# Kernel tuning notes

Hardware: AMD Instinct MI355X
Metric: run time of the kernel (lower is better)

## Reference

```python
import jax, jax.numpy as jnp
import numpy as np

B, NR, IC, NC, OC = 64, 16384, 16, 10, 16
NUM_ITERS = 3


def setup_inputs() -> dict:
    key = jax.random.key(0)
    k1, k2, k3, k4 = jax.random.split(key, 4)
    x = jax.random.normal(k1, (B, NR, IC), dtype=jnp.float32)
    W = jax.random.normal(k2, (IC, NC, OC, NR), dtype=jnp.float32)
    fc_w = jax.random.normal(k3, (1, NC * OC), dtype=jnp.float32)
    fc_b = jax.random.normal(k4, (1,), dtype=jnp.float32)
    return {"x": x, "W": W, "fc_w": fc_w, "fc_b": fc_b}


def _squash(s):
    # Original squash is applied to tensors with trailing dim of size 1,
    # so the norm reduction is elementwise: s^2 * s / ((1+s^2) * sqrt(s^2))
    sq = s * s
    return sq * s / ((1.0 + sq) * jnp.sqrt(sq))


def reference(x, W, fc_w, fc_b):
    batch = x.shape[0]
    in_ch, nc, oc, nr = W.shape
    # u_hat[b,i,c,o] = sum_r W[i,c,o,r] * x[b,r,i]  (x is identical across capsules)
    u_hat = jnp.einsum('icor,bri->bico', W, x)  # [B, in_ch, nc, oc]
    b_ij = jnp.zeros((in_ch, nc), dtype=x.dtype)
    v_j = None
    for it in range(NUM_ITERS):
        c_ij = jax.nn.softmax(b_ij, axis=0)              # softmax over in_channels
        s_j = jnp.einsum('ic,bico->bco', c_ij, u_hat)    # [B, nc, oc]
        v_j = _squash(s_j)
        if it < NUM_ITERS - 1:
            # agreement a[b,i,c] = sum_o u_hat[b,i,c,o] * v[b,c,o]; mean over batch
            a_ij = jnp.einsum('bico,bco->ic', u_hat, v_j) / batch
            b_ij = b_ij + a_ij
    pred = jax.nn.sigmoid(v_j.reshape(batch, -1) @ fc_w.T + fc_b)[:, 0]  # [B]
    return pred, v_j[..., None]  # v_j returned as [B, nc, oc, 1] like torch
```

## Files before the change

kernel.cpp:

```cpp
#include <hip/hip_runtime.h>

typedef unsigned int uint;
typedef unsigned short ushort;
typedef __attribute__((ext_vector_type(8))) short bf16x8;
typedef __attribute__((ext_vector_type(4))) float floatx4;
typedef __attribute__((ext_vector_type(4))) uint uint4v;

#define B_   64
#define NR_  16384
#define IC_  16
#define NC_  10
#define OC_  16
#define NCO  160
#define KC_  32
#define KT_  32

__device__ __forceinline__ float bf2f(ushort h) {
    return __uint_as_float(((uint)h) << 16);
}
__device__ __forceinline__ ushort f2bf(float f) {
    uint u = __float_as_uint(f);
    u += 0x7fffu + ((u >> 16) & 1u);
    return (ushort)(u >> 16);
}
__device__ __forceinline__ void splitbf(float f, ushort& h, ushort& l) {
    h = f2bf(f);
    l = f2bf(f - bf2f(h));
}
__device__ __forceinline__ float squashf(float s) {
    return s * fabsf(s) / (1.0f + s * s);
}

__global__ __launch_bounds__(256) void k_xT(const float* __restrict__ xf,
                                            ushort* __restrict__ xTh,
                                            ushort* __restrict__ xTl)
{
    const int chunk = blockIdx.x, b = blockIdx.y, t = threadIdx.x;
    const int r0 = chunk * 1024;
#pragma unroll
    for (int j = 0; j < 4; ++j) {
        int r = r0 + t + 256 * j;
        const float* row = xf + ((size_t)b * NR_ + r) * IC_;
        float vals[16];
        *(float4*)&vals[0]  = *(const float4*)row;
        *(float4*)&vals[4]  = *(const float4*)(row + 4);
        *(float4*)&vals[8]  = *(const float4*)(row + 8);
        *(float4*)&vals[12] = *(const float4*)(row + 12);
#pragma unroll
        for (int i = 0; i < 16; ++i) {
            ushort h, l;
            splitbf(vals[i], h, l);
            size_t idx = ((size_t)(i * B_ + b)) * NR_ + r;
            xTh[idx] = h;
            xTl[idx] = l;
        }
    }
}

__global__ __launch_bounds__(512) void k_uhat(const float* __restrict__ xf,
                                              const float* __restrict__ wf,
                                              const ushort* __restrict__ xTh,
                                              const ushort* __restrict__ xTl,
                                              int has_xt,
                                              float* __restrict__ uh)
{
    const int i    = blockIdx.x;
    const int kc   = blockIdx.y;
    const int tid  = threadIdx.x;
    const int lane = tid & 63;
    const int w    = tid >> 6;
    const int quad = lane >> 4;
    const int m16  = lane & 15;
    const int bt   = w & 3;
    const int cg   = w >> 2;

    __shared__ ushort Xh[64 * 40], Xl[64 * 40];
    __shared__ ushort Wh[160 * 40], Wl[160 * 40];

    floatx4 acc[5];
#pragma unroll
    for (int t = 0; t < 5; ++t) acc[t] = (floatx4){0.f, 0.f, 0.f, 0.f};

    const int r0 = kc * (NR_ / KC_);

    for (int st = 0; st < (NR_ / KC_) / KT_; ++st) {
        const int rb = r0 + st * KT_;
        __syncthreads();
        if (has_xt) {
            int t8 = tid & 255, bb = t8 >> 2, part = t8 & 3;
            size_t src = (size_t)(i * B_ + bb) * NR_ + rb + part * 8;
            if (tid < 256)
                *(uint4v*)&Xh[bb * 40 + part * 8] = *(const uint4v*)&xTh[src];
            else
                *(uint4v*)&Xl[bb * 40 + part * 8] = *(const uint4v*)&xTl[src];
        } else {
#pragma unroll
            for (int s = 0; s < 4; ++s) {
                int n = tid + 512 * s;
                int bb = n >> 5, k = n & 31;
                float v = xf[(size_t)bb * (NR_ * IC_) + (size_t)(rb + k) * IC_ + i];
                ushort h, l;
                splitbf(v, h, l);
                Xh[bb * 40 + k] = h;
                Xl[bb * 40 + k] = l;
            }
        }
        for (int j = tid; j < 640; j += 512) {
            int row = j >> 2, seg = j & 3;
            const float* wp = wf + (size_t)(i * NCO + row) * NR_ + rb + seg * 8;
            float4 f0 = *(const float4*)wp;
            float4 f1 = *(const float4*)(wp + 4);
            float v[8] = {f0.x, f0.y, f0.z, f0.w, f1.x, f1.y, f1.z, f1.w};
            ushort hh[8], ll[8];
#pragma unroll
            for (int q = 0; q < 8; ++q) splitbf(v[q], hh[q], ll[q]);
            uint4v ph, pl;
#pragma unroll
            for (int q = 0; q < 4; ++q) {
                ph[q] = (uint)hh[2 * q] | ((uint)hh[2 * q + 1] << 16);
                pl[q] = (uint)ll[2 * q] | ((uint)ll[2 * q + 1] << 16);
            }
            *(uint4v*)&Wh[row * 40 + seg * 8] = ph;
            *(uint4v*)&Wl[row * 40 + seg * 8] = pl;
        }
        __syncthreads();
        bf16x8 afh = *(const bf16x8*)&Xh[(bt * 16 + m16) * 40 + quad * 8];
        bf16x8 afl = *(const bf16x8*)&Xl[(bt * 16 + m16) * 40 + quad * 8];
#pragma unroll
        for (int t = 0; t < 5; ++t) {
            int corow = (cg * 5 + t) * 16 + m16;
            bf16x8 bh = *(const bf16x8*)&Wh[corow * 40 + quad * 8];
            bf16x8 bl = *(const bf16x8*)&Wl[corow * 40 + quad * 8];
            acc[t] = __builtin_amdgcn_mfma_f32_16x16x32_bf16(afh, bh, acc[t], 0, 0, 0);
            acc[t] = __builtin_amdgcn_mfma_f32_16x16x32_bf16(afl, bh, acc[t], 0, 0, 0);
            acc[t] = __builtin_amdgcn_mfma_f32_16x16x32_bf16(afh, bl, acc[t], 0, 0, 0);
        }
    }
#pragma unroll
    for (int t = 0; t < 5; ++t) {
        int co = (cg * 5 + t) * 16 + m16;
#pragma unroll
        for (int r = 0; r < 4; ++r) {
            int b = bt * 16 + quad * 4 + r;
            atomicAdd(&uh[(b * IC_ + i) * NCO + co], acc[t][r]);
        }
    }
}

__global__ __launch_bounds__(256) void k_route1(const float* __restrict__ uh,
                                                float* __restrict__ a1)
{
    const int b = blockIdx.x, tid = threadIdx.x;
    __shared__ float vL[NCO];
    const float* ub = uh + b * IC_ * NCO;
    if (tid < NCO) {
        float s = 0.f;
#pragma unroll
        for (int i = 0; i < IC_; ++i) s += ub[i * NCO + tid];
        vL[tid] = squashf(s * (1.0f / 16.0f));
    }
    __syncthreads();
    if (tid < NCO) {
        int i = tid / NC_, c = tid - i * NC_;
        float sum = 0.f;
#pragma unroll
        for (int o = 0; o < OC_; ++o)
            sum += ub[i * NCO + c * OC_ + o] * vL[c * OC_ + o];
        atomicAdd(&a1[i * NC_ + c], sum * (1.0f / 64.0f));
    }
}

__global__ __launch_bounds__(256) void k_route2(const float* __restrict__ uh,
                                                const float* __restrict__ a1,
                                                float* __restrict__ a2)
{
    const int b = blockIdx.x, tid = threadIdx.x;
    __shared__ float aL[NCO];
    __shared__ float vL[NCO];
    if (tid < NCO) aL[tid] = a1[tid];
    __syncthreads();
    const float* ub = uh + b * IC_ * NCO;
    if (tid < NCO) {
        int c = tid >> 4;
        float m = -1e30f;
        for (int i = 0; i < IC_; ++i) m = fmaxf(m, aL[i * NC_ + c]);
        float Z = 0.f;
        for (int i = 0; i < IC_; ++i) Z += expf(aL[i * NC_ + c] - m);
        float s = 0.f;
        for (int i = 0; i < IC_; ++i)
            s += (expf(aL[i * NC_ + c] - m) / Z) * ub[i * NCO + tid];
        vL[tid] = squashf(s);
    }
    __syncthreads();
    if (tid < NCO) {
        int i = tid / NC_, c = tid - i * NC_;
        float sum = 0.f;
#pragma unroll
        for (int o = 0; o < OC_; ++o)
            sum += ub[i * NCO + c * OC_ + o] * vL[c * OC_ + o];
        atomicAdd(&a2[i * NC_ + c], sum * (1.0f / 64.0f));
    }
}

__global__ __launch_bounds__(256) void k_route3(const float* __restrict__ uh,
                                                const float* __restrict__ a1,
                                                const float* __restrict__ a2,
                                                const float* __restrict__ fcw,
                                                const float* __restrict__ fcb,
                                                float* __restrict__ out)
{
    const int b = blockIdx.x, tid = threadIdx.x;
    __shared__ float bL[NCO];
    __shared__ float pL[NCO];
    if (tid < NCO) bL[tid] = a1[tid] + a2[tid];
    __syncthreads();
    const float* ub = uh + b * IC_ * NCO;
    if (tid < NCO) {
        int c = tid >> 4;
        float m = -1e30f;
        for (int i = 0; i < IC_; ++i) m = fmaxf(m, bL[i * NC_ + c]);
        float Z = 0.f;
        for (int i = 0; i < IC_; ++i) Z += expf(bL[i * NC_ + c] - m);
        float s = 0.f;
        for (int i = 0; i < IC_; ++i)
            s += (expf(bL[i * NC_ + c] - m) / Z) * ub[i * NCO + tid];
        float v = squashf(s);
        out[64 + b * NCO + tid] = v;
        pL[tid] = v * fcw[tid];
    }
    __syncthreads();
    if (tid == 0) {
        float accv = fcb[0];
        for (int j = 0; j < NCO; ++j) accv += pL[j];
        out[b] = 1.0f / (1.0f + expf(-accv));
    }
}

extern "C" void kernel_launch(void* const* d_in, const int* in_sizes, int n_in,
                              void* d_out, int out_size, void* d_ws, size_t ws_size,
                              hipStream_t stream)
{
    const float* x   = (const float*)d_in[0];
    const float* W   = (const float*)d_in[1];
    const float* fcw = (const float*)d_in[2];
    const float* fcb = (const float*)d_in[3];
    float* out = (float*)d_out;

    float* uh = (float*)d_ws;
    float* a1 = uh + B_ * IC_ * NCO;
    float* a2 = a1 + NCO;
    const size_t xt_off   = 1u << 20;
    const size_t xt_bytes = (size_t)IC_ * B_ * NR_ * 2;
    ushort* xTh = (ushort*)((char*)d_ws + xt_off);
    ushort* xTl = (ushort*)((char*)d_ws + xt_off + xt_bytes);
    const int has_xt = (ws_size >= xt_off + 2 * xt_bytes) ? 1 : 0;

    hipMemsetAsync(d_ws, 0, (size_t)(B_ * IC_ * NCO + 2 * NCO) * sizeof(float), stream);
    if (has_xt)
        k_xT<<<dim3(16, 64), 256, 0, stream>>>(x, xTh, xTl);
    k_uhat<<<dim3(IC_, KC_), 512, 0, stream>>>(x, W, xTh, xTl, has_xt, uh);
    k_route1<<<B_, 256, 0, stream>>>(uh, a1);
    k_route2<<<B_, 256, 0, stream>>>(uh, a1, a2);
    k_route3<<<B_, 256, 0, stream>>>(uh, a1, a2, fcw, fcb, out);
}
```

Baseline: 320.6 us.

## Replace atomics with partial-sum buffers, widen K tile, vectorize transpose

The u_hat GEMM now writes per-K-chunk partial results to a workspace buffer, and a new reduce kernel sums them instead of using global atomicAdd. The hipMemset is removed. The K tile doubles to 64 with padded shared-memory strides, which halves the loop iterations and barriers. The x transpose kernel now loads four rows per thread and stores packed 8-byte values. The routing kernels stage u_hat in shared memory and compute per-batch agreement partials that are summed on read rather than with atomics. The fallback path for small workspaces is dropped, so the code now assumes a larger workspace (over 100 MB) is available.

New measurement: 324.1 us. Within noise of the previous version (+1.1%).

```diff
diff --git a/kernel.cpp b/kernel.cpp
--- a/kernel.cpp
+++ b/kernel.cpp
@@ -5,6 +5,7 @@
 typedef __attribute__((ext_vector_type(8))) short bf16x8;
 typedef __attribute__((ext_vector_type(4))) float floatx4;
 typedef __attribute__((ext_vector_type(4))) uint uint4v;
+typedef __attribute__((ext_vector_type(2))) uint uint2v;
 
 #define B_   64
 #define NR_  16384
@@ -12,8 +13,9 @@
 #define NC_  10
 #define OC_  16
 #define NCO  160
+#define ICO  2560
 #define KC_  32
-#define KT_  32
+#define KT_  64
 
 __device__ __forceinline__ float bf2f(ushort h) {
     return __uint_as_float(((uint)h) << 16);
@@ -36,33 +38,31 @@
                                             ushort* __restrict__ xTl)
 {
     const int chunk = blockIdx.x, b = blockIdx.y, t = threadIdx.x;
-    const int r0 = chunk * 1024;
-#pragma unroll
-    for (int j = 0; j < 4; ++j) {
-        int r = r0 + t + 256 * j;
-        const float* row = xf + ((size_t)b * NR_ + r) * IC_;
-        float vals[16];
-        *(float4*)&vals[0]  = *(const float4*)row;
-        *(float4*)&vals[4]  = *(const float4*)(row + 4);
-        *(float4*)&vals[8]  = *(const float4*)(row + 8);
-        *(float4*)&vals[12] = *(const float4*)(row + 12);
-#pragma unroll
-        for (int i = 0; i < 16; ++i) {
-            ushort h, l;
-            splitbf(vals[i], h, l);
-            size_t idx = ((size_t)(i * B_ + b)) * NR_ + r;
-            xTh[idx] = h;
-            xTl[idx] = l;
-        }
-    }
-}
-
-__global__ __launch_bounds__(512) void k_uhat(const float* __restrict__ xf,
-                                              const float* __restrict__ wf,
+    const int r0 = chunk * 1024 + t * 4;
+    const float* base = xf + ((size_t)b * NR_ + r0) * IC_;
+    float v[4][16];
+#pragma unroll
+    for (int q = 0; q < 4; ++q)
+#pragma unroll
+        for (int s = 0; s < 4; ++s)
+            *(float4*)&v[q][s * 4] = *(const float4*)(base + q * IC_ + s * 4);
+#pragma unroll
+    for (int i = 0; i < 16; ++i) {
+        ushort h[4], l[4];
+#pragma unroll
+        for (int q = 0; q < 4; ++q) splitbf(v[q][i], h[q], l[q]);
+        size_t idx = ((size_t)(i * B_ + b)) * NR_ + r0;
+        *(uint2v*)&xTh[idx] = (uint2v){(uint)h[0] | ((uint)h[1] << 16),
+                                       (uint)h[2] | ((uint)h[3] << 16)};
+        *(uint2v*)&xTl[idx] = (uint2v){(uint)l[0] | ((uint)l[1] << 16),
+                                       (uint)l[2] | ((uint)l[3] << 16)};
+    }
+}
+
+__global__ __launch_bounds__(512) void k_uhat(const float* __restrict__ wf,
                                               const ushort* __restrict__ xTh,
                                               const ushort* __restrict__ xTl,
-                                              int has_xt,
-                                              float* __restrict__ uh)
+                                              float* __restrict__ up)
 {
     const int i    = blockIdx.x;
     const int kc   = blockIdx.y;
@@ -74,8 +74,8 @@
     const int bt   = w & 3;
     const int cg   = w >> 2;
 
-    __shared__ ushort Xh[64 * 40], Xl[64 * 40];
-    __shared__ ushort Wh[160 * 40], Wl[160 * 40];
+    __shared__ ushort Xh[64 * 72], Xl[64 * 72];
+    __shared__ ushort Wh[160 * 72], Wl[160 * 72];
 
     floatx4 acc[5];
 #pragma unroll
@@ -86,27 +86,14 @@
     for (int st = 0; st < (NR_ / KC_) / KT_; ++st) {
         const int rb = r0 + st * KT_;
         __syncthreads();
-        if (has_xt) {
-            int t8 = tid & 255, bb = t8 >> 2, part = t8 & 3;
-            size_t src = (size_t)(i * B_ + bb) * NR_ + rb + part * 8;
-            if (tid < 256)
-                *(uint4v*)&Xh[bb * 40 + part * 8] = *(const uint4v*)&xTh[src];
-            else
-                *(uint4v*)&Xl[bb * 40 + part * 8] = *(const uint4v*)&xTl[src];
-        } else {
-#pragma unroll
-            for (int s = 0; s < 4; ++s) {
-                int n = tid + 512 * s;
-                int bb = n >> 5, k = n & 31;
-                float v = xf[(size_t)bb * (NR_ * IC_) + (size_t)(rb + k) * IC_ + i];
-                ushort h, l;
-                splitbf(v, h, l);
-                Xh[bb * 40 + k] = h;
-                Xl[bb * 40 + k] = l;
-            }
-        }
-        for (int j = tid; j < 640; j += 512) {
-            int row = j >> 2, seg = j & 3;
+        {
+            int bb = tid >> 3, seg = tid & 7;
+            size_t src = (size_t)(i * B_ + bb) * NR_ + rb + seg * 8;
+            *(uint4v*)&Xh[bb * 72 + seg * 8] = *(const uint4v*)&xTh[src];
+            *(uint4v*)&Xl[bb * 72 + seg * 8] = *(const uint4v*)&xTl[src];
+        }
+        for (int j = tid; j < 1280; j += 512) {
+            int row = j >> 3, seg = j & 7;
             const float* wp = wf + (size_t)(i * NCO + row) * NR_ + rb + seg * 8;
             float4 f0 = *(const float4*)wp;
             float4 f1 = *(const float4*)(wp + 4);
@@ -120,20 +107,23 @@
                 ph[q] = (uint)hh[2 * q] | ((uint)hh[2 * q + 1] << 16);
                 pl[q] = (uint)ll[2 * q] | ((uint)ll[2 * q + 1] << 16);
             }
-            *(uint4v*)&Wh[row * 40 + seg * 8] = ph;
-            *(uint4v*)&Wl[row * 40 + seg * 8] = pl;
+            *(uint4v*)&Wh[row * 72 + seg * 8] = ph;
+            *(uint4v*)&Wl[row * 72 + seg * 8] = pl;
         }
         __syncthreads();
-        bf16x8 afh = *(const bf16x8*)&Xh[(bt * 16 + m16) * 40 + quad * 8];
-        bf16x8 afl = *(const bf16x8*)&Xl[(bt * 16 + m16) * 40 + quad * 8];
-#pragma unroll
-        for (int t = 0; t < 5; ++t) {
-            int corow = (cg * 5 + t) * 16 + m16;
-            bf16x8 bh = *(const bf16x8*)&Wh[corow * 40 + quad * 8];
-            bf16x8 bl = *(const bf16x8*)&Wl[corow * 40 + quad * 8];
-            acc[t] = __builtin_amdgcn_mfma_f32_16x16x32_bf16(afh, bh, acc[t], 0, 0, 0);
-            acc[t] = __builtin_amdgcn_mfma_f32_16x16x32_bf16(afl, bh, acc[t], 0, 0, 0);
-            acc[t] = __builtin_amdgcn_mfma_f32_16x16x32_bf16(afh, bl, acc[t], 0, 0, 0);
+#pragma unroll
+        for (int kk = 0; kk < 2; ++kk) {
+            bf16x8 afh = *(const bf16x8*)&Xh[(bt * 16 + m16) * 72 + kk * 32 + quad * 8];
+            bf16x8 afl = *(const bf16x8*)&Xl[(bt * 16 + m16) * 72 + kk * 32 + quad * 8];
+#pragma unroll
+            for (int t = 0; t < 5; ++t) {
+                int corow = (cg * 5 + t) * 16 + m16;
+                bf16x8 bh = *(const bf16x8*)&Wh[corow * 72 + kk * 32 + quad * 8];
+                bf16x8 bl = *(const bf16x8*)&Wl[corow * 72 + kk * 32 + quad * 8];
+                acc[t] = __builtin_amdgcn_mfma_f32_16x16x32_bf16(afh, bh, acc[t], 0, 0, 0);
+                acc[t] = __builtin_amdgcn_mfma_f32_16x16x32_bf16(afl, bh, acc[t], 0, 0, 0);
+                acc[t] = __builtin_amdgcn_mfma_f32_16x16x32_bf16(afh, bl, acc[t], 0, 0, 0);
+            }
         }
     }
 #pragma unroll
@@ -142,21 +132,33 @@
 #pragma unroll
         for (int r = 0; r < 4; ++r) {
             int b = bt * 16 + quad * 4 + r;
-            atomicAdd(&uh[(b * IC_ + i) * NCO + co], acc[t][r]);
-        }
-    }
-}
-
-__global__ __launch_bounds__(256) void k_route1(const float* __restrict__ uh,
-                                                float* __restrict__ a1)
+            up[((size_t)kc * B_ + b) * ICO + i * NCO + co] = acc[t][r];
+        }
+    }
+}
+
+__global__ __launch_bounds__(256) void k_reduce(const float* __restrict__ up,
+                                                float* __restrict__ uh)
+{
+    const int g = blockIdx.x * 256 + threadIdx.x;
+    float s = 0.f;
+#pragma unroll
+    for (int kc = 0; kc < KC_; ++kc) s += up[(size_t)kc * (B_ * ICO) + g];
+    uh[g] = s;
+}
+
+__global__ __launch_bounds__(256) void k_r1(const float* __restrict__ uh,
+                                            float* __restrict__ a1p)
 {
     const int b = blockIdx.x, tid = threadIdx.x;
+    __shared__ float uhb[ICO];
     __shared__ float vL[NCO];
-    const float* ub = uh + b * IC_ * NCO;
-    if (tid < NCO) {
-        float s = 0.f;
-#pragma unroll
-        for (int i = 0; i < IC_; ++i) s += ub[i * NCO + tid];
+    for (int e = tid; e < ICO; e += 256) uhb[e] = uh[b * ICO + e];
+    __syncthreads();
+    if (tid < NCO) {
+        float s = 0.f;
+#pragma unroll
+        for (int i = 0; i < IC_; ++i) s += uhb[i * NCO + tid];
         vL[tid] = squashf(s * (1.0f / 16.0f));
     }
     __syncthreads();
@@ -165,21 +167,27 @@
         float sum = 0.f;
 #pragma unroll
         for (int o = 0; o < OC_; ++o)
-            sum += ub[i * NCO + c * OC_ + o] * vL[c * OC_ + o];
-        atomicAdd(&a1[i * NC_ + c], sum * (1.0f / 64.0f));
-    }
-}
-
-__global__ __launch_bounds__(256) void k_route2(const float* __restrict__ uh,
-                                                const float* __restrict__ a1,
-                                                float* __restrict__ a2)
+            sum += uhb[i * NCO + c * OC_ + o] * vL[c * OC_ + o];
+        a1p[b * NCO + tid] = sum * (1.0f / 64.0f);
+    }
+}
+
+__global__ __launch_bounds__(256) void k_r2(const float* __restrict__ uh,
+                                            const float* __restrict__ a1p,
+                                            float* __restrict__ a2p)
 {
     const int b = blockIdx.x, tid = threadIdx.x;
+    __shared__ float uhb[ICO];
     __shared__ float aL[NCO];
     __shared__ float vL[NCO];
-    if (tid < NCO) aL[tid] = a1[tid];
-    __syncthreads();
-    const float* ub = uh + b * IC_ * NCO;
+    for (int e = tid; e < ICO; e += 256) uhb[e] = uh[b * ICO + e];
+    if (tid < NCO) {
+        float s = 0.f;
+#pragma unroll
+        for (int b2 = 0; b2 < B_; ++b2) s += a1p[b2 * NCO + tid];
+        aL[tid] = s;
+    }
+    __syncthreads();
     if (tid < NCO) {
         int c = tid >> 4;
         float m = -1e30f;
@@ -188,7 +196,7 @@
         for (int i = 0; i < IC_; ++i) Z += expf(aL[i * NC_ + c] - m);
         float s = 0.f;
         for (int i = 0; i < IC_; ++i)
-            s += (expf(aL[i * NC_ + c] - m) / Z) * ub[i * NCO + tid];
+            s += (expf(aL[i * NC_ + c] - m) / Z) * uhb[i * NCO + tid];
         vL[tid] = squashf(s);
     }
     __syncthreads();
@@ -197,24 +205,31 @@
         float sum = 0.f;
 #pragma unroll
         for (int o = 0; o < OC_; ++o)
-            sum += ub[i * NCO + c * OC_ + o] * vL[c * OC_ + o];
-        atomicAdd(&a2[i * NC_ + c], sum * (1.0f / 64.0f));
-    }
-}
-
-__global__ __launch_bounds__(256) void k_route3(const float* __restrict__ uh,
-                                                const float* __restrict__ a1,
-                                                const float* __restrict__ a2,
-                                                const float* __restrict__ fcw,
-                                                const float* __restrict__ fcb,
-                                                float* __restrict__ out)
+            sum += uhb[i * NCO + c * OC_ + o] * vL[c * OC_ + o];
+        a2p[b * NCO + tid] = sum * (1.0f / 64.0f);
+    }
+}
+
+__global__ __launch_bounds__(256) void k_r3(const float* __restrict__ uh,
+                                            const float* __restrict__ a1p,
+                                            const float* __restrict__ a2p,
+                                            const float* __restrict__ fcw,
+                                            const float* __restrict__ fcb,
+                                            float* __restrict__ out)
 {
     const int b = blockIdx.x, tid = threadIdx.x;
+    __shared__ float uhb[ICO];
     __shared__ float bL[NCO];
     __shared__ float pL[NCO];
-    if (tid < NCO) bL[tid] = a1[tid] + a2[tid];
-    __syncthreads();
-    const float* ub = uh + b * IC_ * NCO;
+    for (int e = tid; e < ICO; e += 256) uhb[e] = uh[b * ICO + e];
+    if (tid < NCO) {
+        float s = 0.f;
+#pragma unroll
+        for (int b2 = 0; b2 < B_; ++b2)
+            s += a1p[b2 * NCO + tid] + a2p[b2 * NCO + tid];
+        bL[tid] = s;
+    }
+    __syncthreads();
     if (tid < NCO) {
         int c = tid >> 4;
         float m = -1e30f;
@@ -223,7 +238,7 @@
         for (int i = 0; i < IC_; ++i) Z += expf(bL[i * NC_ + c] - m);
         float s = 0.f;
         for (int i = 0; i < IC_; ++i)
-            s += (expf(bL[i * NC_ + c] - m) / Z) * ub[i * NCO + tid];
+            s += (expf(bL[i * NC_ + c] - m) / Z) * uhb[i * NCO + tid];
         float v = squashf(s);
         out[64 + b * NCO + tid] = v;
         pL[tid] = v * fcw[tid];
@@ -246,20 +261,18 @@
     const float* fcb = (const float*)d_in[3];
     float* out = (float*)d_out;
 
-    float* uh = (float*)d_ws;
-    float* a1 = uh + B_ * IC_ * NCO;
-    float* a2 = a1 + NCO;
-    const size_t xt_off   = 1u << 20;
-    const size_t xt_bytes = (size_t)IC_ * B_ * NR_ * 2;
-    ushort* xTh = (ushort*)((char*)d_ws + xt_off);
-    ushort* xTl = (ushort*)((char*)d_ws + xt_off + xt_bytes);
-    const int has_xt = (ws_size >= xt_off + 2 * xt_bytes) ? 1 : 0;
-
-    hipMemsetAsync(d_ws, 0, (size_t)(B_ * IC_ * NCO + 2 * NCO) * sizeof(float), stream);
-    if (has_xt)
-        k_xT<<<dim3(16, 64), 256, 0, stream>>>(x, xTh, xTl);
-    k_uhat<<<dim3(IC_, KC_), 512, 0, stream>>>(x, W, xTh, xTl, has_xt, uh);
-    k_route1<<<B_, 256, 0, stream>>>(uh, a1);
-    k_route2<<<B_, 256, 0, stream>>>(uh, a1, a2);
-    k_route3<<<B_, 256, 0, stream>>>(uh, a1, a2, fcw, fcb, out);
-}
+    char* wsb = (char*)d_ws;
+    float*  uh  = (float*)wsb;
+    float*  a1p = (float*)(wsb + 655360);
+    float*  a2p = (float*)(wsb + 696320);
+    ushort* xTh = (ushort*)(wsb + (1u << 20));
+    ushort* xTl = (ushort*)(wsb + (1u << 20) + 33554432u);
+    float*  up  = (float*)(wsb + (1u << 20) + 67108864u);
+
+    k_xT<<<dim3(16, B_), 256, 0, stream>>>(x, xTh, xTl);
+    k_uhat<<<dim3(IC_, KC_), 512, 0, stream>>>(W, xTh, xTl, up);
+    k_reduce<<<(B_ * ICO) / 256, 256, 0, stream>>>(up, uh);
+    k_r1<<<B_, 256, 0, stream>>>(uh, a1p);
+    k_r2<<<B_, 256, 0, stream>>>(uh, a1p, a2p);
+    k_r3<<<B_, 256, 0, stream>>>(uh, a1p, a2p, fcw, fcb, out);
+}
```
